# Optimization experiments

Measured on AMD Instinct MI355X. Metric: run time of the kernel, lower is better.

Reference implementation:

```python
import jax, jax.numpy as jnp
import numpy as np

B, T, D = 4, 2048, 1024  # batch, seq_len, dec_dim_in == dim_proj_QK == dim_proj_V == dec_dim_out


def setup_inputs() -> dict:
    key = jax.random.key(0)
    ks = jax.random.split(key, 9)
    s = 1.0 / np.sqrt(D)  # torch Linear default init scale
    return {
        "x": jax.random.normal(ks[0], (B, T, D), dtype=jnp.float32),
        "Wq": jax.random.uniform(ks[1], (D, D), jnp.float32, -s, s),
        "bq": jax.random.uniform(ks[2], (D,), jnp.float32, -s, s),
        "Wk": jax.random.uniform(ks[3], (D, D), jnp.float32, -s, s),
        "bk": jax.random.uniform(ks[4], (D,), jnp.float32, -s, s),
        "Wv": jax.random.uniform(ks[5], (D, D), jnp.float32, -s, s),
        "bv": jax.random.uniform(ks[6], (D,), jnp.float32, -s, s),
        "Wh": jax.random.uniform(ks[7], (D, D), jnp.float32, -s, s),
        "bh": jax.random.uniform(ks[8], (D,), jnp.float32, -s, s),
    }


def reference(x, Wq, bq, Wk, bk, Wv, bv, Wh, bh):
    Q = x @ Wq + bq                      # [B, T, Dqk]
    K = x @ Wk + bk                      # [B, T, Dqk]
    V = x @ Wv + bv                      # [B, T, Dv]
    scale = 1.0 / jnp.sqrt(jnp.asarray(K.shape[-1], x.dtype))
    scores = jnp.einsum("btd,bsd->bts", Q, K) * scale  # [B, T, T]
    t = K.shape[1]
    causal = jnp.triu(jnp.ones((t, t), dtype=bool), k=1)  # True above diagonal
    scores = jnp.where(causal[None, :, :], -jnp.inf, scores)
    attn = jax.nn.softmax(scores, axis=-1)
    # dropout is identity in eval mode (reference baseline)
    out = jnp.einsum("bts,bsd->btd", attn, V)  # [B, T, Dv]
    return out @ Wh + bh
```

## Files before the change

kernel.cpp:

```cpp
#include <hip/hip_runtime.h>


typedef __attribute__((ext_vector_type(8)))  short short8;
typedef __attribute__((ext_vector_type(4)))  float f4;
typedef __attribute__((ext_vector_type(8)))  unsigned short us8;

#define BM 128
#define BN 128
#define BK 64

__device__ inline unsigned short f2bf(float f) {
    union { float f; unsigned u; } c; c.f = f;
    unsigned u = c.u;
    return (unsigned short)((u + 0x7fffu + ((u >> 16) & 1u)) >> 16);
}
__device__ inline float bf2f(unsigned short u) {
    union { unsigned u; float f; } c; c.u = ((unsigned)u) << 16;
    return c.f;
}
__device__ inline void gload16(const void* g, void* l) {
    __builtin_amdgcn_global_load_lds(
        (const __attribute__((address_space(1))) void*)g,
        (__attribute__((address_space(3))) void*)l,
        16, 0, 0);
}

__global__ __launch_bounds__(256)
void gemm_bt(const unsigned short* __restrict__ A,
             const unsigned short* __restrict__ Bt,
             void* __restrict__ C,
             const float* __restrict__ bias,
             int M, int N, int K, int lda, int ldb, int ldc,
             long sA, long sB, long sC,
             float scale, int flags,
             unsigned short* __restrict__ C2, long sC2, int Tv, int vsplit,
             const float* __restrict__ rowscale)
{
    const int b = blockIdx.z;
    A  += (long)b * sA;
    Bt += (long)b * sB;
    if (flags & 32) rowscale += (long)b * M;

    int by = blockIdx.y;
    if (flags & 8) by = gridDim.y - 1 - by;
    const int m0 = by * BM;
    const int n0 = blockIdx.x * BN;

    if ((flags & 2) && n0 > m0 + (BM - 1)) return;

    int kend = K;
    if (flags & 4) { int ke = m0 + BM; kend = ke < K ? ke : K; }
    const int numK = kend / BK;

    __shared__ unsigned short As[BM * BK];
    __shared__ unsigned short Bs[BN * BK];

    const int tid  = threadIdx.x;
    const int lane = tid & 63;
    const int wave = tid >> 6;
    const int wm   = wave & 1;
    const int wn   = wave >> 1;
    const int lrow = lane & 15;
    const int quad = lane >> 4;

    f4 acc[4][4];
#pragma unroll
    for (int i = 0; i < 4; ++i)
#pragma unroll
        for (int j = 0; j < 4; ++j) acc[i][j] = (f4)0.0f;

    const int srow = tid >> 3;
    const int gco  = ((tid & 7) ^ (srow & 7)) << 3;
    const int rdsl = (lrow & 7);

    for (int kt = 0; kt < numK; ++kt) {
        const int k0 = kt * BK;
#pragma unroll
        for (int d = 0; d < 4; ++d) {
            const int row = d * 32 + srow;
            const unsigned short* ga = A  + (long)(m0 + row) * lda + k0 + gco;
            const unsigned short* gb = Bt + (long)(n0 + row) * ldb + k0 + gco;
            const int ldsoff = (d * 256 + wave * 64) * 16;
            gload16(ga, (char*)As + ldsoff);
            gload16(gb, (char*)Bs + ldsoff);
        }
        __syncthreads();

#pragma unroll
        for (int ks = 0; ks < 2; ++ks) {
            const int slot = ((ks * 4 + quad) ^ rdsl) << 3;
            short8 af[4], bfr[4];
#pragma unroll
            for (int i = 0; i < 4; ++i) {
                af[i]  = *(const short8*)(As + (wm * 64 + i * 16 + lrow) * BK + slot);
                bfr[i] = *(const short8*)(Bs + (wn * 64 + i * 16 + lrow) * BK + slot);
            }
#pragma unroll
            for (int i = 0; i < 4; ++i)
#pragma unroll
                for (int j = 0; j < 4; ++j)
                    acc[i][j] = __builtin_amdgcn_mfma_f32_16x16x32_bf16(
                        af[i], bfr[j], acc[i][j], 0, 0, 0);
        }
        __syncthreads();
    }

    const int row0 = m0 + wm * 64 + quad * 4;
    const int col0 = n0 + wn * 64 + lrow;

    float bj[4];
#pragma unroll
    for (int j = 0; j < 4; ++j) bj[j] = bias ? bias[col0 + j * 16] : 0.0f;

    if ((flags & 16) && n0 >= vsplit) {
        const int bidx  = m0 >> 11;
        const int tloc0 = (m0 & 2047) + wm * 64 + quad * 4;
#pragma unroll
        for (int j = 0; j < 4; ++j) {
            const int d = col0 + j * 16 - vsplit;
            unsigned short* base = C2 + (long)bidx * sC2 + (long)d * Tv;
#pragma unroll
            for (int i = 0; i < 4; ++i) {
                const int tt = tloc0 + i * 16;
                unsigned long long pk = 0;
#pragma unroll
                for (int r = 0; r < 4; ++r) {
                    float v = acc[i][j][r] * scale + bj[j];
                    pk |= (unsigned long long)f2bf(v) << (16 * r);
                }
                *(unsigned long long*)(base + tt) = pk;
            }
        }
        return;
    }

    const bool obf = flags & 1;
    unsigned short* Cb = (unsigned short*)C;
    float*          Cf = (float*)C;
    const long cbase = (long)b * sC;

#pragma unroll
    for (int i = 0; i < 4; ++i) {
#pragma unroll
        for (int j = 0; j < 4; ++j) {
            const int col = col0 + j * 16;
#pragma unroll
            for (int r = 0; r < 4; ++r) {
                const int row = row0 + i * 16 + r;
                float v = acc[i][j][r] * scale + bj[j];
                if (flags & 64) { v = __expf(v); if (col > row) v = 0.0f; }
                if (flags & 32) v *= rowscale[row];
                const long off = cbase + (long)row * ldc + col;
                if (obf) Cb[off] = f2bf(v);
                else     Cf[off] = v;
            }
        }
    }
}

__global__ void rowsum(const unsigned short* __restrict__ P,
                       float* __restrict__ invl, int T)
{
    const int t = blockIdx.x;
    const long rowoff = ((long)blockIdx.y * T + t) * T;
    const int L = t + 1;
    const int tid = threadIdx.x;
    const int lane = tid & 63, wave = tid >> 6;
    __shared__ float red[4];

    us8 raw = *(const us8*)(P + rowoff + tid * 8);
    const int i0 = tid * 8;
    float sum = 0.0f;
#pragma unroll
    for (int k = 0; k < 8; ++k)
        if (i0 + k < L) sum += bf2f(raw[k]);
    for (int o = 32; o > 0; o >>= 1) sum += __shfl_down(sum, o);
    if (lane == 0) red[wave] = sum;
    __syncthreads();
    if (tid == 0) {
        sum = red[0] + red[1] + red[2] + red[3];
        invl[(long)blockIdx.y * T + t] = 1.0f / sum;
    }
}

__global__ void prep(const float* __restrict__ x,
                     const float* __restrict__ Wq, const float* __restrict__ Wk,
                     const float* __restrict__ Wv, const float* __restrict__ Wh,
                     const float* __restrict__ bq, const float* __restrict__ bk,
                     const float* __restrict__ bv,
                     unsigned short* __restrict__ Xbf,
                     unsigned short* __restrict__ Wqkvt,
                     unsigned short* __restrict__ Wht,
                     float* __restrict__ bqkv)
{
    typedef __attribute__((ext_vector_type(4))) float f4v;
    __shared__ unsigned short tsh[32][33];
    const int bid = blockIdx.x;
    const int tid = threadIdx.x;

    if (bid < 8192) {
        const int i = bid * 256 + tid;
        f4v v = ((const f4v*)x)[i];
        unsigned long long p = (unsigned long long)f2bf(v.x)
                             | ((unsigned long long)f2bf(v.y) << 16)
                             | ((unsigned long long)f2bf(v.z) << 32)
                             | ((unsigned long long)f2bf(v.w) << 48);
        ((unsigned long long*)Xbf)[i] = p;
    } else if (bid < 12288) {
        const int wi = bid - 8192;
        const int w = wi >> 10, tile = wi & 1023;
        const float* src = (w == 0) ? Wq : (w == 1) ? Wk : (w == 2) ? Wv : Wh;
        unsigned short* dst = (w < 3) ? (Wqkvt + (size_t)w * 1024 * 1024) : Wht;
        const int c0 = (tile & 31) * 32, r0 = (tile >> 5) * 32;
        const int xx = tid & 31, yy = tid >> 5;
        for (int i = yy; i < 32; i += 8)
            tsh[i][xx] = f2bf(src[(long)(r0 + i) * 1024 + c0 + xx]);
        __syncthreads();
        for (int i = yy; i < 32; i += 8)
            dst[(long)(c0 + i) * 1024 + r0 + xx] = tsh[xx][i];
    } else {
        const int i = (bid - 12288) * 256 + tid;
        if (i < 1024) { bqkv[i] = bq[i]; bqkv[1024 + i] = bk[i]; bqkv[2048 + i] = bv[i]; }
    }
}

extern "C" void kernel_launch(void* const* d_in, const int* in_sizes, int n_in,
                              void* d_out, int out_size, void* d_ws, size_t ws_size,
                              hipStream_t stream)
{
    const float* x  = (const float*)d_in[0];
    const float* Wq = (const float*)d_in[1];
    const float* bq = (const float*)d_in[2];
    const float* Wk = (const float*)d_in[3];
    const float* bk = (const float*)d_in[4];
    const float* Wv = (const float*)d_in[5];
    const float* bv = (const float*)d_in[6];
    const float* Wh = (const float*)d_in[7];
    const float* bh = (const float*)d_in[8];
    float* out = (float*)d_out;

    const int  Bb = 4, T = 2048, Dm = 1024;
    const long BT = (long)Bb * T;

    unsigned short* ws = (unsigned short*)d_ws;
    size_t o = 0;
    unsigned short* Xbf   = ws + o; o += (size_t)BT * Dm;
    unsigned short* Wqkvt = ws + o; o += (size_t)3 * Dm * Dm;
    unsigned short* Wht   = ws + o; o += (size_t)Dm * Dm;
    float* bqkv = (float*)(ws + o); o += (size_t)3 * Dm * 2;
    unsigned short* QKV   = ws + o; o += (size_t)BT * 3 * Dm;
    unsigned short* Vt    = ws + o; o += (size_t)BT * Dm;
    unsigned short* Pp    = ws + o; o += (size_t)Bb * T * T;
    float* invlb = (float*)(ws + o); o += (size_t)BT * 2;
    unsigned short* Ob    = ws + o;

    const dim3 blk(256);
    const long sRow3 = (long)T * 3 * Dm;

    prep<<<12292, blk, 0, stream>>>(x, Wq, Wk, Wv, Wh, bq, bk, bv,
                                    Xbf, Wqkvt, Wht, bqkv);

    gemm_bt<<<dim3(3 * Dm / BN, BT / BM, 1), blk, 0, stream>>>(
        Xbf, Wqkvt, QKV, bqkv, (int)BT, 3 * Dm, Dm, Dm, Dm, 3 * Dm,
        0, 0, 0, 1.0f, 1 | 16, Vt, (long)Dm * T, T, 2 * Dm, nullptr);

    gemm_bt<<<dim3(T / BN, T / BM, Bb), blk, 0, stream>>>(
        QKV, QKV + Dm, Pp, nullptr, T, T, Dm, 3 * Dm, 3 * Dm, T,
        sRow3, sRow3, (long)T * T, 1.0f / 32.0f, 1 | 2 | 8 | 64,
        nullptr, 0, 0, 0, nullptr);

    rowsum<<<dim3(T, Bb), blk, 0, stream>>>(Pp, invlb, T);

    gemm_bt<<<dim3(Dm / BN, T / BM, Bb), blk, 0, stream>>>(
        Pp, Vt, Ob, nullptr, T, Dm, T, T, T, Dm,
        (long)T * T, (long)Dm * T, (long)T * Dm, 1.0f, 1 | 4 | 8 | 32,
        nullptr, 0, 0, 0, invlb);

    gemm_bt<<<dim3(Dm / BN, BT / BM, 1), blk, 0, stream>>>(
        Ob, Wht, out, bh, (int)BT, Dm, Dm, Dm, Dm, Dm,
        0, 0, 0, 1.0f, 0, nullptr, 0, 0, 0, nullptr);
}
```

Measured before the change: 320.9 us.

## Fold output projection into V weights by precomputing Wv·Wh and fused bias

The output projection is folded into the value projection: Wv@Wh is computed once as a small 1024^3 GEMM, and the bias becomes bv@Wh + bh, computed with a GEMV. The PV GEMM then writes the final fp32 output directly, adding the folded bias after the 1/l row scaling. This removes the separate 8192x1024x1024 output GEMM and the bf16 intermediate O buffer. In exchange it adds a 1024^3 GEMM, a GEMV, and an extra rounding of the folded weight product to bf16.

```diff
diff --git a/kernel.cpp b/kernel.cpp
--- a/kernel.cpp
+++ b/kernel.cpp
@@ -147,9 +147,10 @@
 #pragma unroll
             for (int r = 0; r < 4; ++r) {
                 const int row = row0 + i * 16 + r;
-                float v = acc[i][j][r] * scale + bj[j];
+                float v = acc[i][j][r] * scale;
                 if (flags & 64) { v = __expf(v); if (col > row) v = 0.0f; }
                 if (flags & 32) v *= rowscale[row];
+                v += bj[j];
                 const long off = cbase + (long)row * ldc + col;
                 if (obf) Cb[off] = f2bf(v);
                 else     Cf[off] = v;
@@ -183,14 +184,36 @@
     }
 }
 
+__global__ void gemv_bhh(const unsigned short* __restrict__ Wht,
+                         const float* __restrict__ bv,
+                         const float* __restrict__ bh,
+                         float* __restrict__ bhh)
+{
+    const int m = blockIdx.x;
+    const int tid = threadIdx.x;
+    const int lane = tid & 63, wave = tid >> 6;
+    __shared__ float red[4];
+    const unsigned short* row = Wht + (long)m * 1024;
+    float s = 0.0f;
+#pragma unroll
+    for (int k = 0; k < 4; ++k) {
+        const int idx = tid * 4 + k;
+        s += bf2f(row[idx]) * bv[idx];
+    }
+    for (int o = 32; o > 0; o >>= 1) s += __shfl_down(s, o);
+    if (lane == 0) red[wave] = s;
+    __syncthreads();
+    if (tid == 0) bhh[m] = red[0] + red[1] + red[2] + red[3] + bh[m];
+}
+
 __global__ void prep(const float* __restrict__ x,
                      const float* __restrict__ Wq, const float* __restrict__ Wk,
                      const float* __restrict__ Wv, const float* __restrict__ Wh,
                      const float* __restrict__ bq, const float* __restrict__ bk,
-                     const float* __restrict__ bv,
                      unsigned short* __restrict__ Xbf,
                      unsigned short* __restrict__ Wqkvt,
                      unsigned short* __restrict__ Wht,
+                     unsigned short* __restrict__ Wvb,
                      float* __restrict__ bqkv)
 {
     typedef __attribute__((ext_vector_type(4))) float f4v;
@@ -206,11 +229,19 @@
                              | ((unsigned long long)f2bf(v.z) << 32)
                              | ((unsigned long long)f2bf(v.w) << 48);
         ((unsigned long long*)Xbf)[i] = p;
+    } else if (bid < 9216) {
+        const int i = (bid - 8192) * 256 + tid;
+        f4v v = ((const f4v*)Wv)[i];
+        unsigned long long p = (unsigned long long)f2bf(v.x)
+                             | ((unsigned long long)f2bf(v.y) << 16)
+                             | ((unsigned long long)f2bf(v.z) << 32)
+                             | ((unsigned long long)f2bf(v.w) << 48);
+        ((unsigned long long*)Wvb)[i] = p;
     } else if (bid < 12288) {
-        const int wi = bid - 8192;
+        const int wi = bid - 9216;
         const int w = wi >> 10, tile = wi & 1023;
-        const float* src = (w == 0) ? Wq : (w == 1) ? Wk : (w == 2) ? Wv : Wh;
-        unsigned short* dst = (w < 3) ? (Wqkvt + (size_t)w * 1024 * 1024) : Wht;
+        const float* src = (w == 0) ? Wq : (w == 1) ? Wk : Wh;
+        unsigned short* dst = (w == 0) ? Wqkvt : (w == 1) ? (Wqkvt + 1024 * 1024) : Wht;
         const int c0 = (tile & 31) * 32, r0 = (tile >> 5) * 32;
         const int xx = tid & 31, yy = tid >> 5;
         for (int i = yy; i < 32; i += 8)
@@ -220,7 +251,7 @@
             dst[(long)(c0 + i) * 1024 + r0 + xx] = tsh[xx][i];
     } else {
         const int i = (bid - 12288) * 256 + tid;
-        if (i < 1024) { bqkv[i] = bq[i]; bqkv[1024 + i] = bk[i]; bqkv[2048 + i] = bv[i]; }
+        if (i < 1024) { bqkv[i] = bq[i]; bqkv[1024 + i] = bk[i]; bqkv[2048 + i] = 0.0f; }
     }
 }
 
@@ -247,18 +278,25 @@
     unsigned short* Xbf   = ws + o; o += (size_t)BT * Dm;
     unsigned short* Wqkvt = ws + o; o += (size_t)3 * Dm * Dm;
     unsigned short* Wht   = ws + o; o += (size_t)Dm * Dm;
+    unsigned short* Wvb   = ws + o; o += (size_t)Dm * Dm;
     float* bqkv = (float*)(ws + o); o += (size_t)3 * Dm * 2;
+    float* bhh  = (float*)(ws + o); o += (size_t)Dm * 2;
     unsigned short* QKV   = ws + o; o += (size_t)BT * 3 * Dm;
     unsigned short* Vt    = ws + o; o += (size_t)BT * Dm;
     unsigned short* Pp    = ws + o; o += (size_t)Bb * T * T;
     float* invlb = (float*)(ws + o); o += (size_t)BT * 2;
-    unsigned short* Ob    = ws + o;
 
     const dim3 blk(256);
     const long sRow3 = (long)T * 3 * Dm;
 
-    prep<<<12292, blk, 0, stream>>>(x, Wq, Wk, Wv, Wh, bq, bk, bv,
-                                    Xbf, Wqkvt, Wht, bqkv);
+    prep<<<12289, blk, 0, stream>>>(x, Wq, Wk, Wv, Wh, bq, bk,
+                                    Xbf, Wqkvt, Wht, Wvb, bqkv);
+
+    gemm_bt<<<dim3(Dm / BN, Dm / BM, 1), blk, 0, stream>>>(
+        Wht, Wvb, Wqkvt + 2 * Dm * Dm, nullptr, Dm, Dm, Dm, Dm, Dm, Dm,
+        0, 0, 0, 1.0f, 1, nullptr, 0, 0, 0, nullptr);
+
+    gemv_bhh<<<Dm, blk, 0, stream>>>(Wht, bv, bh, bhh);
 
     gemm_bt<<<dim3(3 * Dm / BN, BT / BM, 1), blk, 0, stream>>>(
         Xbf, Wqkvt, QKV, bqkv, (int)BT, 3 * Dm, Dm, Dm, Dm, 3 * Dm,
@@ -272,11 +310,7 @@
     rowsum<<<dim3(T, Bb), blk, 0, stream>>>(Pp, invlb, T);
 
     gemm_bt<<<dim3(Dm / BN, T / BM, Bb), blk, 0, stream>>>(
-        Pp, Vt, Ob, nullptr, T, Dm, T, T, T, Dm,
-        (long)T * T, (long)Dm * T, (long)T * Dm, 1.0f, 1 | 4 | 8 | 32,
+        Pp, Vt, out, bhh, T, Dm, T, T, T, Dm,
+        (long)T * T, (long)Dm * T, (long)T * Dm, 1.0f, 4 | 8 | 32,
         nullptr, 0, 0, 0, invlb);
-
-    gemm_bt<<<dim3(Dm / BN, BT / BM, 1), blk, 0, stream>>>(
-        Ob, Wht, out, bh, (int)BT, Dm, Dm, Dm, Dm, Dm,
-        0, 0, 0, 1.0f, 0, nullptr, 0, 0, 0, nullptr);
-}
+}
```

New measurement: 318.0 us. Within noise of the previous version (-0.9%).
